# Kernel optimization log

Hardware: AMD Instinct MI355X
Metric: run time of the kernel (lower is better)

## Reference

```python
import jax, jax.numpy as jnp
import numpy as np

N_NODES, NUM_FEAT, EMB, HID, N_CLASSES, N_EDGES = 800, 111, 32, 200, 15, 8000
ALPHA = 0.5   # DirGNNConv default mixing
EPS = 1e-5    # LayerNorm eps


def _pade_coeffs(deg=5):
    # [5/5] Pade approximant of sqrt(1 - x) (as in FastDifferentiableMatSqrt)
    K = 2 * deg + 1
    b = np.zeros(K); b[0] = 1.0
    for k in range(1, K):
        b[k] = b[k - 1] * (0.5 - (k - 1)) / k
    c = b * ((-1.0) ** np.arange(K))  # Taylor coeffs of sqrt(1-x)
    A = np.empty((deg, deg))
    for i in range(deg):
        for j in range(1, deg + 1):
            A[i, j - 1] = c[deg + 1 + i - j]
    q = np.concatenate([[1.0], np.linalg.solve(A, -c[deg + 1:])])
    p = np.array([sum(q[j] * c[k - j] for j in range(min(k, deg) + 1)) for k in range(deg + 1)])
    return p.astype(np.float32), q.astype(np.float32)

PADE_P, PADE_Q = _pade_coeffs()


def _mpa_impl(A):
    # matrix square root via Pade approximant (MPA forward)
    normA = jnp.sqrt(jnp.sum(A * A))
    I = jnp.eye(A.shape[0], dtype=A.dtype)
    p_app = I - A / normA
    p_hat = p_app
    p_sqrt = PADE_P[0] * I
    q_sqrt = PADE_Q[0] * I
    for i in range(5):
        p_sqrt = p_sqrt + PADE_P[i + 1] * p_hat
        q_sqrt = q_sqrt + PADE_Q[i + 1] * p_hat
        p_hat = p_hat @ p_app
    return jnp.linalg.solve(q_sqrt, p_sqrt) * jnp.sqrt(normA)


@jax.custom_vjp
def mpa_lya(A):
    return _mpa_impl(A)


def _mpa_fwd(A):
    S = _mpa_impl(A)
    return S, (S, jnp.sqrt(jnp.sum(A * A)))


def _mpa_bwd(res, g):
    # iterative Lyapunov solver backward (8 coupled Newton-Schulz iterations)
    S, normA = res
    I = jnp.eye(S.shape[0], dtype=S.dtype)
    b = S / jnp.sqrt(normA)
    c = g / jnp.sqrt(normA)
    for _ in range(8):
        b2 = b @ b
        c = 0.5 * (c @ (3.0 * I - b2) - b2 @ c + b @ (c @ b))
        b = 0.5 * (b @ (3.0 * I - b2))
    return (0.5 * c,)

mpa_lya.defvjp(_mpa_fwd, _mpa_bwd)


def gcn_sparse(m, ei, n):
    # GCNConv(normalize=False): out[dst] = sum_{(src,dst) in E} (x @ W)[src]
    return jax.ops.segment_sum(m[ei[0]], ei[1], num_segments=n)


def hetero_layer_sparse(h, eis, W, b):
    # W: [3(in,out,root), 4 edge types, Fin, Fout]; HeteroConv aggr='sum'
    n = h.shape[0]
    out = jnp.zeros((n, W.shape[-1]), h.dtype)
    for e, ei in enumerate(eis):
        x_in = gcn_sparse(h @ W[0, e], ei, n) + b[0, e]
        x_out = gcn_sparse(h @ W[1, e], ei[::-1], n) + b[1, e]  # flipped edges
        out = out + ALPHA * x_out + (1.0 - ALPHA) * x_in + h @ W[2, e] + b[2, e]
    return out


def hetero_layer_dense(h, masks, W, b):
    # masks: [4, N, N] binary adjacency (src, dst); dense equivalent of scatter
    out = jnp.zeros((h.shape[0], W.shape[-1]), h.dtype)
    for e in range(masks.shape[0]):
        x_in = masks[e].T @ (h @ W[0, e]) + b[0, e]
        x_out = masks[e] @ (h @ W[1, e]) + b[1, e]
        out = out + ALPHA * x_out + (1.0 - ALPHA) * x_in + h @ W[2, e] + b[2, e]
    return out


def graph_layernorm(h, wb):
    # PyG LayerNorm mode='graph', single graph: normalize over all nodes+feats
    mu = jnp.mean(h)
    var = jnp.mean((h - mu) ** 2)
    return (h - mu) / jnp.sqrt(var + EPS) * wb[0] + wb[1]


def hetero_gnn(h, layer_fn, graph, W1, b1, W2, b2, ln):
    h = graph_layernorm(layer_fn(h, graph, W1, b1), ln[0])
    return graph_layernorm(layer_fn(h, graph, W2, b2), ln[1])


def pairwise_S(z, lin_W, lin_b, iu, ju):
    n = z.shape[0]
    M = (z[iu] - z[ju]) ** 2                        # [N(N+1)/2, HID]
    mg = jax.nn.sigmoid(M @ lin_W + lin_b)[:, 0]    # upper-tri entries, row-major
    tri = jnp.zeros((n, n), z.dtype).at[iu, ju].set(mg)
    return mpa_lya(tri)


def model_forward(x_note, embed_W, embed_b, g1_l1_W, g1_l1_b, g1_l2_W, g1_l2_b, g1_ln,
                  g2_l1_W, g2_l1_b, g2_l2_W, g2_l2_b, g2_ln, lin_W, lin_b, clf_W, clf_b,
                  eis, batch):
    n = x_note.shape[0]
    iu, ju = np.triu_indices(n)
    h = x_note @ embed_W + embed_b                   # [N, 32]
    z0 = hetero_gnn(h, hetero_layer_sparse, eis, g1_l1_W, g1_l1_b, g1_l2_W, g1_l2_b, g1_ln)
    S1 = pairwise_S(z0, lin_W, lin_b, iu, ju)
    A0 = jnp.stack([jnp.zeros((n, n), h.dtype).at[ei[0], ei[1]].set(1.0) for ei in eis])
    h = S1 @ h
    # adj_to_coord(nonzero) only keeps the binary pattern of S1 @ A @ S1
    mask1 = jnp.stack([((S1 @ A0[e]) @ S1 != 0).astype(h.dtype) for e in range(4)])
    z1 = hetero_gnn(h, hetero_layer_dense, mask1, g2_l1_W, g2_l1_b, g2_l2_W, g2_l2_b, g2_ln)
    S2 = pairwise_S(z1, lin_W, lin_b, iu, ju)
    h = S2 @ h
    mask2 = jnp.stack([((S2 @ mask1[e]) @ S2 != 0).astype(h.dtype) for e in range(4)])
    z2 = hetero_gnn(h, hetero_layer_dense, mask2, g2_l1_W, g2_l1_b, g2_l2_W, g2_l2_b, g2_ln)
    counts = jax.ops.segment_sum(jnp.ones((n,), z2.dtype), batch, num_segments=1)
    x2 = jax.ops.segment_sum(z2, batch, num_segments=1) / counts[:, None]  # global_mean_pool
    logits = x2 @ clf_W + clf_b
    return x2, jax.nn.log_softmax(logits, axis=-1), S1, S2


def setup_inputs() -> dict:
    key = jax.random.key(0)
    ks = jax.random.split(key, 14)
    N, F, E, H, NC, NE = N_NODES, NUM_FEAT, EMB, HID, N_CLASSES, N_EDGES
    def w(k, shape, fan_in):
        return (jax.random.normal(k, shape, jnp.float32) / np.sqrt(fan_in)).astype(jnp.float32)
    ln = jnp.broadcast_to(jnp.stack([jnp.ones(H, jnp.float32), jnp.zeros(H, jnp.float32)]), (2, 2, H)) + 0.0
    return dict(
        x_note=jax.random.normal(ks[0], (N, F), jnp.float32),
        embed_W=w(ks[1], (F, E), F), embed_b=jnp.zeros((E,), jnp.float32),
        g1_l1_W=w(ks[2], (3, 4, E, H), E), g1_l1_b=jnp.zeros((3, 4, H), jnp.float32),
        g1_l2_W=w(ks[3], (3, 4, H, H), H), g1_l2_b=jnp.zeros((3, 4, H), jnp.float32),
        g1_ln=ln,
        g2_l1_W=w(ks[4], (3, 4, E, H), E), g2_l1_b=jnp.zeros((3, 4, H), jnp.float32),
        g2_l2_W=w(ks[5], (3, 4, H, H), H), g2_l2_b=jnp.zeros((3, 4, H), jnp.float32),
        g2_ln=ln,
        lin_W=w(ks[6], (H, 1), H), lin_b=jnp.zeros((1,), jnp.float32),
        clf_W=w(ks[7], (H, NC), H), clf_b=jnp.zeros((NC,), jnp.float32),
        ei_forward=jax.random.randint(ks[8], (2, NE), 0, N, jnp.int32),
        ei_onset=jax.random.randint(ks[9], (2, NE), 0, N, jnp.int32),
        ei_sustain=jax.random.randint(ks[10], (2, NE), 0, N, jnp.int32),
        ei_rest=jax.random.randint(ks[11], (2, NE), 0, N, jnp.int32),
        batch=jnp.zeros((N,), jnp.int32),
    )


def reference(x_note, embed_W, embed_b, g1_l1_W, g1_l1_b, g1_l2_W, g1_l2_b, g1_ln,
              g2_l1_W, g2_l1_b, g2_l2_W, g2_l2_b, g2_ln, lin_W, lin_b, clf_W, clf_b,
              ei_forward, ei_onset, ei_sustain, ei_rest, batch):
    eis = (ei_forward, ei_onset, ei_sustain, ei_rest)
    return model_forward(x_note, embed_W, embed_b, g1_l1_W, g1_l1_b, g1_l2_W, g1_l2_b, g1_ln,
                         g2_l1_W, g2_l1_b, g2_l2_W, g2_l2_b, g2_ln, lin_W, lin_b, clf_W, clf_b,
                         eis, batch)
```

## Files before the change

### kernel.cpp

```cpp
#include <hip/hip_runtime.h>
#include <hip/hip_bf16.h>
#include <math.h>
#include <stdio.h>

static constexpr int   kN  = 800;
static constexpr int   kF  = 111;
static constexpr int   kE  = 32;
static constexpr int   kH  = 200;
static constexpr int   kNC = 15;
static constexpr int   kNE = 8000;
static constexpr long  kNN = (long)kN*kN;
static constexpr long  kNH = (long)kN*kH;
static constexpr float kAl  = 0.5f;
static constexpr float kEps = 1e-5f;
static constexpr int   kGB  = (int)((kNH+255)/256);
static constexpr int   kDB  = 50;
static constexpr int   kCH  = 50;
static constexpr int   kNCHK= kN/kCH;

typedef unsigned short u16;
typedef __attribute__((ext_vector_type(8))) short short8;
typedef __attribute__((ext_vector_type(4))) float f32x4;

__device__ __forceinline__ u16 f2bf(float v){
  __hip_bfloat16 b = __float2bfloat16(v);
  return *reinterpret_cast<u16*>(&b);
}
__device__ __forceinline__ float bf2f(u16 h){
  unsigned int u = ((unsigned int)h) << 16;
  float f; __builtin_memcpy(&f, &u, 4);
  return f;
}

enum { EPI_NONE=0, EPI_BIAS=1, EPI_SCALE=4, EPI_ACC=6 };

template<bool TRANSA, bool TRIUA, bool TRIUB, int EPI, bool LNA>
__global__ __launch_bounds__(256)
void gemm_kernel(const float* __restrict__ A, int lda,
                 const float* __restrict__ B, int ldb,
                 float* __restrict__ C, int ldc,
                 int M, int Ncl, int K,
                 long sA, long sB, long sC, float scale,
                 const float* __restrict__ bias, int kstep,
                 const double* __restrict__ scalp,
                 const float* __restrict__ lnw,
                 const double* __restrict__ lnpart, int lnnb)
{
  constexpr int TM=64, TN=64, TK=16;
  A += (long)blockIdx.z * sA;
  B += (long)blockIdx.z * sB;
  C += (long)blockIdx.z * sC;
  __shared__ float As[TK][TM+4];
  __shared__ float Bs[TK][TN+4];
  const int tid = threadIdx.x;
  const int tn4 = (tid & 15)*4, tm4 = (tid >> 4)*4;
  const int m0 = blockIdx.x * TM, n0 = blockIdx.y * TN;
  float acc[4][4] = {};
  float mu = 0.f, rsf = 1.f;
  if (LNA){
    __shared__ double lnS[256], lnQ[256];
    double s=0.0, q=0.0;
    for (int i=tid; i<lnnb; i+=256){ s += lnpart[2*i]; q += lnpart[2*i+1]; }
    lnS[tid]=s; lnQ[tid]=q;
    __syncthreads();
    for (int h=128; h>0; h>>=1){
      if (tid < h){ lnS[tid]+=lnS[tid+h]; lnQ[tid]+=lnQ[tid+h]; }
      __syncthreads();
    }
    double m = lnS[0]/(double)kNH;
    double var = lnQ[0]/(double)kNH - m*m;
    mu = (float)m;
    rsf = rsqrtf((float)var + kEps);
    __syncthreads();
  }
  const int kbase = kstep ? (int)blockIdx.z * kstep : 0;
  int k0 = TRIUA ? max(m0 - kbase, 0) : 0;
  int kEnd = TRIUB ? min(K, n0 + TN - kbase) : K;
  const bool skip = (k0 >= kEnd);
  if (skip && EPI == EPI_ACC) return;
  if (!skip) {
    float ar[4], br[4];
    auto loadT = [&](int kk0, float* arr, float* brr){
      #pragma unroll
      for (int u=0; u<4; ++u){
        int idx = tid + 256*u;
        float av = 0.f;
        if (!TRANSA) {
          int m = idx >> 4, ka = idx & 15;
          int gm = m0+m, gk = kk0+ka;
          if (gm < M && gk < K){
            av = A[(long)gm*lda + gk];
            if (LNA) av = (av - mu)*(rsf*lnw[gk]) + lnw[kH + gk];
          }
        } else {
          int ka = idx >> 6, m = idx & 63;
          int gm = m0+m, gk = kk0+ka;
          if (gm < M && gk < K){
            av = A[(long)gk*lda + gm];
            if (LNA) av = (av - mu)*(rsf*lnw[gk]) + lnw[kH + gk];
          }
        }
        int kb = idx >> 6, nb = idx & 63;
        int gk = kk0+kb, gn = n0+nb;
        arr[u] = av;
        brr[u] = (gk < K && gn < Ncl) ? B[(long)gk*ldb + gn] : 0.f;
      }
    };
    auto storeT = [&](const float* arr, const float* brr){
      #pragma unroll
      for (int u=0; u<4; ++u){
        int idx = tid + 256*u;
        if (!TRANSA){ int m = idx>>4, ka = idx&15; As[ka][m] = arr[u]; }
        else        { int ka = idx>>6, m = idx&63; As[ka][m] = arr[u]; }
        int kb = idx>>6, nb = idx&63;
        Bs[kb][nb] = brr[u];
      }
    };
    loadT(k0, ar, br);
    for (;;){
      __syncthreads();
      storeT(ar, br);
      __syncthreads();
      int kn = k0 + TK;
      bool more = kn < kEnd;
      if (more) loadT(kn, ar, br);
      #pragma unroll
      for (int kk=0; kk<TK; ++kk) {
        float a[4], b[4];
        #pragma unroll
        for (int u=0;u<4;++u){ a[u]=As[kk][tm4+u]; b[u]=Bs[kk][tn4+u]; }
        #pragma unroll
        for (int i=0;i<4;++i)
          #pragma unroll
          for (int j=0;j<4;++j)
            acc[i][j] = fmaf(a[i], b[j], acc[i][j]);
      }
      if (!more) break;
      k0 = kn;
    }
  }
  float sc = scale;
  if (EPI == EPI_ACC && scalp) sc *= (float)sqrt(sqrt(scalp[0]));
  #pragma unroll
  for (int i=0;i<4;++i) {
    int gm = m0 + tm4 + i;
    if (gm >= M) continue;
    #pragma unroll
    for (int j=0;j<4;++j) {
      int gn = n0 + tn4 + j;
      if (gn >= Ncl) continue;
      float v = acc[i][j];
      long off = (long)gm*ldc + gn;
      if (EPI == EPI_BIAS)       C[off] = v + bias[gn];
      else if (EPI == EPI_SCALE) C[off] = scale*v;
      else if (EPI == EPI_ACC)   unsafeAtomicAdd(&C[off], sc*v);
      else                       C[off] = v;
    }
  }
}

template<bool TRANSA, bool TRIUA, bool TRIUB, int EPI, bool LNA = false>
static inline void launch_gemm(hipStream_t st,
                               const float* A, int lda, const float* B, int ldb,
                               float* C, int ldc, int M, int Ncl, int K, int batch,
                               long sA, long sB, long sC, float scale,
                               const float* bias = nullptr, int kstep = 0,
                               const double* scalp = nullptr,
                               const float* lnw = nullptr,
                               const double* lnpart = nullptr, int lnnb = 0)
{
  dim3 grid((M+63)/64, (Ncl+63)/64, batch);
  gemm_kernel<TRANSA,TRIUA,TRIUB,EPI,LNA><<<grid, 256, 0, st>>>(
      A,lda,B,ldb,C,ldc,M,Ncl,K,sA,sB,sC,scale,bias,kstep,scalp,lnw,lnpart,lnnb);
}

__global__ __launch_bounds__(256)
void bgemm2_kernel(const u16* __restrict__ Ah, const u16* __restrict__ Al,
                   const u16* __restrict__ Bh, const u16* __restrict__ Bl,
                   float* __restrict__ C, float* __restrict__ C2,
                   u16* __restrict__ Oh, u16* __restrict__ Ol,
                   float p0, float p1)
{
  constexpr int TM=64, TN=64, BK=32;
  __shared__ u16 Ash[TM][40], Asl[TM][40], Bsh[TN][40], Bsl[TN][40];
  const int tid = threadIdx.x;
  const int m0 = blockIdx.x*TM, n0 = blockIdx.y*TN;
  const int w = tid>>6, lane = tid&63;
  const int wm = (w&1)*32, wn = (w>>1)*32;
  const int quad = lane>>4, lm = lane&15;
  f32x4 acc00={}, acc01={}, acc10={}, acc11={};
  const bool skip = (m0 > n0 + TN - 1);
  int k0 = m0;
  const int kEnd = min(kN, n0+TN);
  const int ar = tid>>2, ac = (tid&3)*8;
  if (!skip){
    uint4 avh, avl, bvh, bvl;
    auto loadT = [&](int kk0){
      avh = {0,0,0,0}; avl = {0,0,0,0}; bvh = {0,0,0,0}; bvl = {0,0,0,0};
      int gk = kk0 + ac;
      if (m0+ar < kN && gk < kN){
        avh = *(const uint4*)(Ah + (long)(m0+ar)*kN + gk);
        avl = *(const uint4*)(Al + (long)(m0+ar)*kN + gk);
      }
      if (n0+ar < kN && gk < kN){
        bvh = *(const uint4*)(Bh + (long)(n0+ar)*kN + gk);
        bvl = *(const uint4*)(Bl + (long)(n0+ar)*kN + gk);
      }
    };
    loadT(k0);
    for (;;){
      __syncthreads();
      *(uint4*)&Ash[ar][ac] = avh; *(uint4*)&Asl[ar][ac] = avl;
      *(uint4*)&Bsh[ar][ac] = bvh; *(uint4*)&Bsl[ar][ac] = bvl;
      __syncthreads();
      int kn = k0 + BK;
      bool more = kn < kEnd;
      if (more) loadT(kn);
      short8 a0h = *(const short8*)&Ash[wm+lm][quad*8];
      short8 a1h = *(const short8*)&Ash[wm+16+lm][quad*8];
      short8 a0l = *(const short8*)&Asl[wm+lm][quad*8];
      short8 a1l = *(const short8*)&Asl[wm+16+lm][quad*8];
      short8 b0h = *(const short8*)&Bsh[wn+lm][quad*8];
      short8 b1h = *(const short8*)&Bsh[wn+16+lm][quad*8];
      short8 b0l = *(const short8*)&Bsl[wn+lm][quad*8];
      short8 b1l = *(const short8*)&Bsl[wn+16+lm][quad*8];
      acc00 = __builtin_amdgcn_mfma_f32_16x16x32_bf16(a0h,b0h,acc00,0,0,0);
      acc00 = __builtin_amdgcn_mfma_f32_16x16x32_bf16(a0h,b0l,acc00,0,0,0);
      acc00 = __builtin_amdgcn_mfma_f32_16x16x32_bf16(a0l,b0h,acc00,0,0,0);
      acc01 = __builtin_amdgcn_mfma_f32_16x16x32_bf16(a0h,b1h,acc01,0,0,0);
      acc01 = __builtin_amdgcn_mfma_f32_16x16x32_bf16(a0h,b1l,acc01,0,0,0);
      acc01 = __builtin_amdgcn_mfma_f32_16x16x32_bf16(a0l,b1h,acc01,0,0,0);
      acc10 = __builtin_amdgcn_mfma_f32_16x16x32_bf16(a1h,b0h,acc10,0,0,0);
      acc10 = __builtin_amdgcn_mfma_f32_16x16x32_bf16(a1h,b0l,acc10,0,0,0);
      acc10 = __builtin_amdgcn_mfma_f32_16x16x32_bf16(a1l,b0h,acc10,0,0,0);
      acc11 = __builtin_amdgcn_mfma_f32_16x16x32_bf16(a1h,b1h,acc11,0,0,0);
      acc11 = __builtin_amdgcn_mfma_f32_16x16x32_bf16(a1h,b1l,acc11,0,0,0);
      acc11 = __builtin_amdgcn_mfma_f32_16x16x32_bf16(a1l,b1h,acc11,0,0,0);
      if (!more) break;
      k0 = kn;
    }
  }
  f32x4 accs[2][2] = {{acc00, acc01},{acc10, acc11}};
  #pragma unroll
  for (int ti=0; ti<2; ++ti){
    #pragma unroll
    for (int tj=0; tj<2; ++tj){
      #pragma unroll
      for (int r=0; r<4; ++r){
        int gm = m0 + wm + ti*16 + quad*4 + r;
        int gn = n0 + wn + tj*16 + lm;
        if (gm >= kN || gn >= kN) continue;
        float v = accs[ti][tj][r];
        long off = (long)gm*kN + gn;
        C[off]  += p0*v;
        C2[off] += p1*v;
        u16 h = f2bf(v);
        Oh[off] = h;
        Ol[off] = f2bf(v - bf2f(h));
      }
    }
  }
}

__global__ __launch_bounds__(256)
void ln_pair_prep_kernel(const float* __restrict__ tnh, const double* __restrict__ part,
                         int nb, const float* __restrict__ ln, const float* __restrict__ linW,
                         u16* __restrict__ zwh, u16* __restrict__ zwl,
                         u16* __restrict__ zzh, u16* __restrict__ zzl,
                         float* __restrict__ avec)
{
  __shared__ double ss[256], qq[256];
  __shared__ float ared[256];
  const int n = blockIdx.x, t = threadIdx.x;
  double s=0.0, q=0.0;
  for (int i=t; i<nb; i+=256){ s += part[2*i]; q += part[2*i+1]; }
  ss[t]=s; qq[t]=q;
  __syncthreads();
  for (int h=128; h>0; h>>=1){
    if (t < h){ ss[t]+=ss[t+h]; qq[t]+=qq[t+h]; }
    __syncthreads();
  }
  double m = ss[0]/(double)kNH;
  const float mu = (float)m;
  const float rs = rsqrtf((float)(qq[0]/(double)kNH - m*m) + kEps);
  float acc = 0.f;
  if (t < kH){
    float z = (tnh[(long)n*kH + t] - mu)*(rs*ln[t]) + ln[kH + t];
    float wv = linW[t];
    float zw = wv*z;
    long off = (long)n*kH + t;
    u16 h1 = f2bf(zw);
    zwh[off] = h1; zwl[off] = f2bf(zw - bf2f(h1));
    u16 h2 = f2bf(z);
    zzh[off] = h2; zzl[off] = f2bf(z - bf2f(h2));
    acc = zw*z;
  }
  ared[t] = acc;
  __syncthreads();
  for (int h=128; h>0; h>>=1){
    if (t < h) ared[t] += ared[t+h];
    __syncthreads();
  }
  if (t == 0) avec[n] = ared[0];
}

__global__ __launch_bounds__(256)
void bgemm_pair_kernel(const u16* __restrict__ Ah, const u16* __restrict__ Al,
                       const u16* __restrict__ Bh, const u16* __restrict__ Bl,
                       const float* __restrict__ avec, const float* __restrict__ linb,
                       float* __restrict__ tri, double* __restrict__ frob2)
{
  constexpr int TM=64, TN=64, BK=32, KK=kH;
  __shared__ u16 Ash[TM][40], Asl[TM][40], Bsh[TN][40], Bsl[TN][40];
  __shared__ float red[256];
  const int tid = threadIdx.x;
  const int m0 = blockIdx.x*TM, n0 = blockIdx.y*TN;
  if (m0 > n0 + TN - 1){
    for (int idx = tid; idx < TM*TN; idx += 256){
      int r = idx >> 6, c = idx & 63;
      int gm = m0 + r, gn = n0 + c;
      if (gm < kN && gn < kN) tri[(long)gm*kN + gn] = 0.f;
    }
    return;
  }
  const int w = tid>>6, lane = tid&63;
  const int wm = (w&1)*32, wn = (w>>1)*32;
// ... 50 lines not shown
        if (gm >= kN || gn >= kN) continue;
        float t = 0.f;
        if (gm <= gn){
          float marg = avec[gm] + avec[gn] - 2.f*accs[ti][tj][r] + lb;
          t = 1.f/(1.f + expf(-marg));
        }
        tri[(long)gm*kN + gn] = t;
        r2 += t*t;
      }
    }
  }
  red[tid] = r2;
  __syncthreads();
  for (int h=128; h>0; h>>=1){
    if (tid < h) red[tid] += red[tid+h];
    __syncthreads();
  }
  if (tid == 0) unsafeAtomicAdd(frob2, (double)red[0]);
}

__global__ __launch_bounds__(256)
void pade_both_kernel(const float* __restrict__ tri, const double* __restrict__ frob2,
                      u16* __restrict__ ph, u16* __restrict__ pl,
                      u16* __restrict__ th, u16* __restrict__ tl,
                      float* __restrict__ psq, float* __restrict__ qsq,
                      float P0, float P1, float Q0, float Q1)
{
  __shared__ float t[32][33];
  const float rn = (float)(1.0 / sqrt(frob2[0]));
  int r0 = blockIdx.y*32, c0 = blockIdx.x*32;
  int tr = threadIdx.x>>5, tc = threadIdx.x&31;
  for (int i=tr; i<32; i+=8){
    int r = r0+i, c = c0+tc;
    float eye = (r==c) ? 1.f : 0.f;
    float pa = eye - tri[(long)r*kN + c]*rn;
    t[i][tc] = pa;
    long off = (long)r*kN + c;
    psq[off] = P0*eye + P1*pa;
    qsq[off] = Q0*eye + Q1*pa;
    u16 h = f2bf(pa);
    ph[off] = h;
    pl[off] = f2bf(pa - bf2f(h));
  }
  __syncthreads();
  for (int i=tr; i<32; i+=8){
    int c = c0+i, r = r0+tc;
    float v = t[tc][i];
    u16 h = f2bf(v);
    th[(long)c*kN + r] = h;
    tl[(long)c*kN + r] = f2bf(v - bf2f(h));
  }
}

__global__ __launch_bounds__(256)
void copy_scale_kernel(const float* __restrict__ src, const double* __restrict__ frob2,
                       float* __restrict__ dst)
{
  const float fac = (float)sqrt(sqrt(frob2[0]));
  long i = (long)blockIdx.x*256 + threadIdx.x;
  if (i < kNN) __builtin_nontemporal_store(src[i]*fac, &dst[i]);
}

__global__ void edge_count_kernel(const int* __restrict__ e0, const int* __restrict__ e1,
                                  const int* __restrict__ e2, const int* __restrict__ e3,
                                  int* __restrict__ cnt){
  const int* eis[4] = {e0,e1,e2,e3};
  const int e = blockIdx.y;
  const int* ei = eis[e];
  int j = blockIdx.x*256 + threadIdx.x;
  if (j >= kNE) return;
  int s = ei[j], d = ei[kNE + j];
  atomicAdd(&cnt[e*kN + d], 1);
  atomicAdd(&cnt[(4+e)*kN + s], 1);
}

__global__ void csr_scan_kernel(const int* __restrict__ cnt, int* __restrict__ offs,
                                int* __restrict__ cur){
  const int l = blockIdx.x;
  if (threadIdx.x != 0) return;
  int acc = 0;
  for (int i = 0; i < kN; ++i){
    offs[l*(kN+1) + i] = acc;
    cur[l*kN + i] = acc;
    acc += cnt[l*kN + i];
  }
  offs[l*(kN+1) + kN] = acc;
}

__global__ void edge_fill_kernel(const int* __restrict__ e0, const int* __restrict__ e1,
                                 const int* __restrict__ e2, const int* __restrict__ e3,
                                 int* __restrict__ cur, int* __restrict__ adj){
  const int* eis[4] = {e0,e1,e2,e3};
  const int e = blockIdx.y;
  const int* ei = eis[e];
  int j = blockIdx.x*256 + threadIdx.x;
  if (j >= kNE) return;
  int s = ei[j], d = ei[kNE + j];
  int p = atomicAdd(&cur[e*kN + d], 1);
  adj[(long)e*kNE + p] = s;
  int q = atomicAdd(&cur[(4+e)*kN + s], 1);
  adj[(long)(4+e)*kNE + q] = d;
}

__global__ __launch_bounds__(256)
void gather_sparse_kernel(const float* __restrict__ Y, const int* __restrict__ offs,
                          const int* __restrict__ adj, const float* __restrict__ bsum,
                          float* __restrict__ tnh, double* __restrict__ part){
  __shared__ double ss[256], qq[256];
  const int n = blockIdx.x;
  const int f = threadIdx.x;
  double sp = 0.0, qp = 0.0;
  float acc = 0.f;
  if (f < kH){
    #pragma unroll
    for (int l = 0; l < 8; ++l){
      const float* Yp = Y + (long)l*kNH;
      int b = offs[l*(kN+1) + n], e2 = offs[l*(kN+1) + n + 1];
      for (int idx = b; idx < e2; ++idx){
        int m = adj[(long)l*kNE + idx];
        acc += Yp[(long)m*kH + f];
      }
    }
    float t = Y[(long)8*kNH + (long)n*kH + f] + bsum[f] + 0.5f*acc;
    tnh[(long)n*kH + f] = t;
    sp = t; qp = (double)t*t;
  }
  ss[threadIdx.x]=sp; qq[threadIdx.x]=qp;
  __syncthreads();
  for (int hh=128; hh>0; hh>>=1){
    if ((int)threadIdx.x < hh){ ss[threadIdx.x]+=ss[threadIdx.x+hh]; qq[threadIdx.x]+=qq[threadIdx.x+hh]; }
    __syncthreads();
  }
  if (threadIdx.x==0){ part[2*blockIdx.x]=ss[0]; part[2*blockIdx.x+1]=qq[0]; }
}

__global__ void edge_gmax_kernel(const int* __restrict__ e0, const int* __restrict__ e1,
                                 const int* __restrict__ e2, const int* __restrict__ e3,
                                 int* __restrict__ g){
  const int* eis[4] = {e0,e1,e2,e3};
  const int e = blockIdx.y;
  const int* ei = eis[e];
  int j = blockIdx.x*256 + threadIdx.x;
  if (j >= kNE) return;
  int s = ei[j], d = ei[kNE + j];
  atomicMax(&g[e*kN + d], s);
}

__global__ __launch_bounds__(256)
void scan_gh_kernel(int* __restrict__ g, int* __restrict__ h){
  __shared__ int gs[kN];
  const int e = blockIdx.x;
  for (int i = threadIdx.x; i < kN; i += 256) gs[i] = g[e*kN + i];
  __syncthreads();
  if (threadIdx.x == 0){
    int m = -1;
    for (int i = 0; i < kN; ++i){ m = max(m, gs[i]); gs[i] = m; }
  }
  __syncthreads();
  for (int i = threadIdx.x; i < kN; i += 256) g[e*kN + i] = gs[i];
  for (int d = threadIdx.x; d < kN; d += 256){
    int lo = 0, hi = kN;
    while (lo < hi){ int mid = (lo+hi)>>1; if (gs[mid] >= d) hi = mid; else lo = mid+1; }
    h[e*kN + d] = lo;
  }
}

__global__ __launch_bounds__(256)
void scan_chunk_kernel(float* __restrict__ Y, float* __restrict__ Tot){
  const int plane = blockIdx.y;
  const int chunk = blockIdx.x;
  const int f = threadIdx.x;
  if (f >= kH) return;
  float* P = Y + (long)plane*kNH + (long)chunk*kCH*kH + f;
  float acc = 0.f;
  if (plane < 4){
    for (int i0 = 0; i0 < kCH; i0 += 5){
      float v0 = P[(long)(i0+0)*kH], v1 = P[(long)(i0+1)*kH], v2 = P[(long)(i0+2)*kH],
            v3 = P[(long)(i0+3)*kH], v4 = P[(long)(i0+4)*kH];
      acc += v0; P[(long)(i0+0)*kH] = acc;
      acc += v1; P[(long)(i0+1)*kH] = acc;
      acc += v2; P[(long)(i0+2)*kH] = acc;
      acc += v3; P[(long)(i0+3)*kH] = acc;
      acc += v4; P[(long)(i0+4)*kH] = acc;
    }
  } else {
    for (int i0 = kCH-1; i0 >= 4; i0 -= 5){
      float v0 = P[(long)(i0-0)*kH], v1 = P[(long)(i0-1)*kH], v2 = P[(long)(i0-2)*kH],
            v3 = P[(long)(i0-3)*kH], v4 = P[(long)(i0-4)*kH];
      acc += v0; P[(long)(i0-0)*kH] = acc;
      acc += v1; P[(long)(i0-1)*kH] = acc;
      acc += v2; P[(long)(i0-2)*kH] = acc;
      acc += v3; P[(long)(i0-3)*kH] = acc;
      acc += v4; P[(long)(i0-4)*kH] = acc;
    }
  }
  Tot[((long)plane*kNCHK + chunk)*kH + f] = acc;
}

__global__ __launch_bounds__(256)
void gather_dense_kernel(const float* __restrict__ Y, const int* __restrict__ g,
                         const int* __restrict__ h, const float* __restrict__ bsum,
                         const float* __restrict__ Tot,
                         float* __restrict__ tnh, double* __restrict__ part){
  __shared__ double ss[256], qq[256];
  long idx = (long)blockIdx.x*256 + threadIdx.x;
  double s = 0.0, q = 0.0;
  if (idx < kNH){
    int n = (int)(idx / kH), f = (int)(idx % kH);
    float v = 0.f;
    #pragma unroll
    for (int e = 0; e < 4; ++e){
      int gi = g[e*kN + n];
      if (gi >= 0){
        v += Y[(long)e*kNH + (long)gi*kH + f];
        int cg = (int)((unsigned)gi / (unsigned)kCH);
        const float* T = Tot + (long)e*kNCHK*kH + f;
        for (int cc = 0; cc < cg; ++cc) v += T[(long)cc*kH];
      }
      int hi = h[e*kN + n];
      if (hi < kN){
        v += Y[(long)(4+e)*kNH + (long)hi*kH + f];
        int ch = (int)((unsigned)hi / (unsigned)kCH);
        const float* T = Tot + (long)(4+e)*kNCHK*kH + f;
        for (int cc = ch+1; cc < kNCHK; ++cc) v += T[(long)cc*kH];
      }
    }
    float t = Y[(long)8*kNH + idx] + bsum[f] + 0.5f*v;
    tnh[idx] = t;
    s = t; q = (double)t*t;
  }
  ss[threadIdx.x]=s; qq[threadIdx.x]=q;
  __syncthreads();
  for (int hh=128; hh>0; hh>>=1){
    if ((int)threadIdx.x < hh){ ss[threadIdx.x]+=ss[threadIdx.x+hh]; qq[threadIdx.x]+=qq[threadIdx.x+hh]; }
    __syncthreads();
  }
  if (threadIdx.x==0){ part[2*blockIdx.x]=ss[0]; part[2*blockIdx.x+1]=qq[0]; }
}

__global__ void sum_root_kernel(const float* __restrict__ W, const float* __restrict__ b,
                                int K, float* __restrict__ Wr, float* __restrict__ bsum){
  int idx = blockIdx.x*256 + threadIdx.x;
  int tot = K*kH;
  if (idx < tot){
    float v = 0.f;
    #pragma unroll
    for (int e=0;e<4;++e) v += W[(long)(8+e)*tot + idx];
    Wr[idx] = v;
  }
  if (idx < kH){
    float v = 0.f;
    #pragma unroll
    for (int e=0;e<4;++e)
      v += (1.f-kAl)*b[(0*4+e)*kH + idx] + kAl*b[(1*4+e)*kH + idx] + b[(2*4+e)*kH + idx];
    bsum[idx] = v;
  }
}

__global__ __launch_bounds__(64)
void invdiag_kernel(const float* __restrict__ U, float* __restrict__ W){
  __shared__ float Us[kDB][kDB+1];
  __shared__ float Xs[kDB][kDB+1];
  const int base = blockIdx.x * kDB;
  const int tid = threadIdx.x;
  for (int idx = tid; idx < kDB*kDB; idx += 64){
    int r = idx / kDB, c = idx % kDB;
    Us[r][c] = U[(long)(base+r)*kN + base + c];
  }
  __syncthreads();
  const int c = tid;
  for (int i = kDB-1; i >= 0; --i){
    if (c < kDB){
      float x;
      if (c < i) x = 0.f;
      else {
        float s = 0.f;
        for (int k = i+1; k < kDB; ++k) s = fmaf(Us[i][k], Xs[k][c], s);
        x = (((c==i)?1.f:0.f) - s) / Us[i][i];
      }
      Xs[i][c] = x;
    }
    __syncthreads();
  }
  for (int idx = tid; idx < kDB*kDB; idx += 64){
    int r = idx / kDB, cc = idx % kDB;
    W[(long)(base+r)*kN + base + cc] = Xs[r][cc];
  }
}

template<int S>
__global__ __launch_bounds__(256)
void merge_fused_kernel(const float* __restrict__ U, float* __restrict__ W){
  __shared__ float Us[S][S+1];
  __shared__ float Wb[S][S+1];
  __shared__ float T[S][S+1];
  const long base = (long)blockIdx.x * (2*S) * (kN+1);
  const int tid = threadIdx.x;
  for (int idx = tid; idx < S*S; idx += 256){
    int r = idx / S, c = idx % S;
    Us[r][c] = U[base + (long)r*kN + S + c];
    Wb[r][c] = W[base + (long)(S+r)*kN + S + c];
  }
  __syncthreads();
  for (int idx = tid; idx < S*S; idx += 256){
    int r = idx / S, c = idx % S;
    float s = 0.f;
    for (int k = 0; k <= c; ++k) s = fmaf(Us[r][k], Wb[k][c], s);
    T[r][c] = s;
  }
// ... 164 lines not shown
  double* scald = (double*)d_ws;
  double* partd = (double*)((char*)d_ws + 512);
  float *h0=ws+o_h0, *h1=ws+o_h1, *h2=ws+o_h2, *tnh=ws+o_tnh,
        *big=ws+o_big, *tri=ws+o_tri, *Sacc=ws+o_sacc, *winv=ws+o_winv,
        *psq=ws+o_psq, *qsq=ws+o_qsq;
  u16* zwh = (u16*)(ws + o_pp);
  u16* zwl = zwh + kNH;
  u16* zzh = zwl + kNH;
  u16* zzl = zzh + kNH;
  float* avec = ws + o_av;
  int* gArr = (int*)(ws + o_g);
  int* hArr = (int*)(ws + o_hh);
  float *wc1=ws+o_wc1, *wc2=ws+o_wc2, *wc3=ws+o_wc3, *wc4=ws+o_wc4, *bs=ws+o_bs;
  int* cntA = (int*)(ws + o_cnt);
  int* offsA= (int*)(ws + o_offs);
  int* curA = (int*)(ws + o_cur);
  int* adjA = (int*)(ws + o_adj);
  u16* papp_h = (u16*)big;
  u16* papp_l = papp_h + kNN;
  u16* pT_h   = papp_l + kNN;
  u16* pT_l   = pT_h + kNN;
  u16* pwA_h  = pT_l + kNN;
  u16* pwA_l  = pwA_h + kNN;
  u16* pwB_h  = pwA_l + kNN;
  u16* pwB_l  = pwB_h + kNN;
  float* totbuf  = big + (long)9*kNH;
  float* colpart = totbuf + (long)8*kNCHK*kH;

  float P[6], Q[6];
  pade_coeffs(P, Q);

  auto eg = [](long n){ return dim3((unsigned)((n+255)/256)); };

  auto layer_gemm = [&](const float* hin, int K, const float* wcat,
                        const float* lnp, int nb){
    if (lnp)
      launch_gemm<false,false,false,EPI_NONE,true>(stream, hin, K, wcat, kH, big, kH,
          kN, kH, K, 9, 0, (long)K*kH, kNH, 0.f, nullptr, 0, nullptr, lnp, partd, nb);
    else
      launch_gemm<false,false,false,EPI_NONE>(stream, hin, K, wcat, kH, big, kH,
          kN, kH, K, 9, 0, (long)K*kH, kNH, 0.f);
  };
  auto sparse_layer = [&](const float* hin, int K, const float* wcat, const float* bsum,
                          const float* lnp, int nb){
    layer_gemm(hin, K, wcat, lnp, nb);
    gather_sparse_kernel<<<dim3(kN),256,0,stream>>>(big, offsA, adjA, bsum, tnh, partd);
  };
  auto dense_layer = [&](const float* hin, int K, const float* wcat, const float* bsum,
                         const float* lnp, int nb){
    layer_gemm(hin, K, wcat, lnp, nb);
    scan_chunk_kernel<<<dim3(kNCHK,8),256,0,stream>>>(big, totbuf);
    gather_dense_kernel<<<kGB,256,0,stream>>>(big, gArr, hArr, bsum, totbuf, tnh, partd);
  };
  auto blocked_trsm = [&](){
    hipMemsetAsync(winv, 0, (size_t)kNN*sizeof(float), stream);
    invdiag_kernel<<<dim3(kN/kDB),64,0,stream>>>(qsq, winv);
    merge_fused_kernel<50><<<dim3(kN/100),256,0,stream>>>(qsq, winv);
    {
      int s = 100, npairs = 4;
      long step = (long)2*s*kN + 2*s;
      launch_gemm<false,false,true,EPI_NONE>(stream,
          qsq + s, kN, winv + (long)s*kN + s, kN, tri, s,
          s, s, s, npairs, step, step, (long)s*s, 0.f);
      launch_gemm<false,true,false,EPI_SCALE>(stream,
          winv, kN, tri, s, winv + s, kN,
          s, s, s, npairs, step, (long)s*s, step, -1.f);
    }
    {
      int s = 200, npairs = 2;
      long step = (long)2*s*kN + 2*s;
      launch_gemm<false,false,true,EPI_NONE>(stream,
          qsq + s, kN, winv + (long)s*kN + s, kN, tri, s,
          s, s, s, npairs, step, step, (long)s*s, 0.f);
      launch_gemm<false,true,false,EPI_SCALE>(stream,
          winv, kN, tri, s, winv + s, kN,
          s, s, s, npairs, step, (long)s*s, step, -1.f);
    }
    {
      hipMemsetAsync(tri, 0, (size_t)400*400*sizeof(float), stream);
      launch_gemm<false,false,true,EPI_ACC>(stream,
          qsq + 400, kN, winv + (long)400*kN + 400, kN, tri, 400,
          400, 400, 100, 4, 100, (long)100*kN, 0, 1.f, nullptr, 100);
      launch_gemm<false,true,false,EPI_ACC>(stream,
          winv, kN, tri, 400, winv + 400, kN,
          400, 400, 100, 4, 100, (long)100*400, 0, -1.f, nullptr, 100);
    }
    hipMemsetAsync(Sacc, 0, (size_t)kNN*sizeof(float), stream);
    launch_gemm<false,true,true,EPI_ACC>(stream,
        winv, kN, psq, kN, Sacc, kN, kN, kN, 100, 8,
        100, (long)100*kN, 0, 1.f, nullptr, 100);
  };
  auto run_pair_mpa = [&](int nb, const float* lnp, float* SoutDst){
    hipMemsetAsync((char*)d_ws + 24, 0, 8, stream);
    ln_pair_prep_kernel<<<dim3(kN),256,0,stream>>>(tnh, partd, nb, lnp, linW,
                                                   zwh, zwl, zzh, zzl, avec);
    bgemm_pair_kernel<<<dim3(13,13),256,0,stream>>>(zwh, zwl, zzh, zzl, avec, linb,
                                                    tri, scald+3);
    pade_both_kernel<<<dim3(25,25),256,0,stream>>>(tri, scald+3, papp_h, papp_l, pT_h, pT_l,
                                                   psq, qsq, P[0],P[1],Q[0],Q[1]);
    dim3 g13(13,13,1);
    bgemm2_kernel<<<g13,256,0,stream>>>(papp_h,papp_l, pT_h,pT_l, psq,qsq, pwA_h,pwA_l, P[2],Q[2]);
    bgemm2_kernel<<<g13,256,0,stream>>>(pwA_h,pwA_l,  pT_h,pT_l, psq,qsq, pwB_h,pwB_l, P[3],Q[3]);
    bgemm2_kernel<<<g13,256,0,stream>>>(pwB_h,pwB_l,  pT_h,pT_l, psq,qsq, pwA_h,pwA_l, P[4],Q[4]);
    bgemm2_kernel<<<g13,256,0,stream>>>(pwA_h,pwA_l,  pT_h,pT_l, psq,qsq, pwB_h,pwB_l, P[5],Q[5]);
    blocked_trsm();
    copy_scale_kernel<<<eg(kNN),256,0,stream>>>(Sacc, scald+3, SoutDst);
  };
  auto s_times_h = [&](const float* hin, float* hout){
    hipMemsetAsync(hout, 0, (size_t)kN*kE*sizeof(float), stream);
    launch_gemm<false,true,false,EPI_ACC>(stream,
        Sacc, kN, hin, kE, hout, kE, kN, kE, 100, 8,
        100, (long)100*kE, 0, 1.f, nullptr, 100, scald+3);
  };

  float* S1f = out + 215;
  float* S2f = out + 215 + kNN;

  hipMemsetAsync(gArr, 0xFF, (size_t)(4*kN)*sizeof(int), stream);
  edge_gmax_kernel<<<dim3((kNE+255)/256,4),256,0,stream>>>(e0,e1,e2,e3, gArr);
  scan_gh_kernel<<<4,256,0,stream>>>(gArr, hArr);
  hipMemsetAsync(cntA, 0, (size_t)(8*kN)*sizeof(int), stream);
  edge_count_kernel<<<dim3((kNE+255)/256,4),256,0,stream>>>(e0,e1,e2,e3, cntA);
  csr_scan_kernel<<<8,64,0,stream>>>(cntA, offsA, curA);
  edge_fill_kernel<<<dim3((kNE+255)/256,4),256,0,stream>>>(e0,e1,e2,e3, curA, adjA);
  hipMemcpyAsync(wc1, g1w1, 8L*kE*kH*sizeof(float), hipMemcpyDeviceToDevice, stream);
  hipMemcpyAsync(wc2, g1w2, 8L*kH*kH*sizeof(float), hipMemcpyDeviceToDevice, stream);
  hipMemcpyAsync(wc3, g2w1, 8L*kE*kH*sizeof(float), hipMemcpyDeviceToDevice, stream);
  hipMemcpyAsync(wc4, g2w2, 8L*kH*kH*sizeof(float), hipMemcpyDeviceToDevice, stream);
  sum_root_kernel<<<eg((long)kE*kH),256,0,stream>>>(g1w1, g1b1, kE, wc1 + 8L*kE*kH, bs);
  sum_root_kernel<<<eg((long)kH*kH),256,0,stream>>>(g1w2, g1b2, kH, wc2 + 8L*kH*kH, bs+kH);
  sum_root_kernel<<<eg((long)kE*kH),256,0,stream>>>(g2w1, g2b1, kE, wc3 + 8L*kE*kH, bs+2*kH);
  sum_root_kernel<<<eg((long)kH*kH),256,0,stream>>>(g2w2, g2b2, kH, wc4 + 8L*kH*kH, bs+3*kH);

  launch_gemm<false,false,false,EPI_BIAS>(stream, x_note, kF, embW, kE, h0, kE, kN, kE, kF, 1,
                                          0,0,0, 0.f, embB);

  sparse_layer(h0,  kE, wc1, bs,      nullptr, 0);
  sparse_layer(tnh, kH, wc2, bs+kH,   g1ln, kN);

  run_pair_mpa(kN, g1ln + 2*kH, S1f);

  s_times_h(h0, h1);

  dense_layer(h1,  kE, wc3, bs+2*kH, nullptr, 0);
  dense_layer(tnh, kH, wc4, bs+3*kH, g2ln, kGB);

  run_pair_mpa(kGB, g2ln + 2*kH, S2f);

  s_times_h(h1, h2);

  dense_layer(h2,  kE, wc3, bs+2*kH, nullptr, 0);
  dense_layer(tnh, kH, wc4, bs+3*kH, g2ln, kGB);

  colsum_kernel<<<dim3(50),256,0,stream>>>(tnh, colpart);
  pool_head_kernel<<<dim3(1),256,0,stream>>>(colpart, partd, kGB, g2ln + 2*kH, clfW, clfb, out);
}
```

Before: 1.068 ms.

## Fuse setup kernels, drop memsets, and replace split-K atomics with direct GEMM stores

Merges weight copies, root-weight sums, bias combining and buffer initialisation into one prep kernel. The edge count and gmax kernels become one, and the two scans become one. Split-K atomic GEMMs in the triangular solve and S·h products become single-pass GEMMs with plain or scaled stores, so their memsets go away. The final S GEMM writes both the raw and scaled outputs, which removes the copy-scale kernel and the unused last bf16 split store. Together this cuts kernel launches and atomic traffic, but each single-pass GEMM now has fewer blocks and so less parallelism. The winv memset is hoisted to run once, which relies on its zero regions never being written in between.

```diff
diff --git a/kernel.cpp b/kernel.cpp
--- a/kernel.cpp
+++ b/kernel.cpp
@@ -32,7 +32,7 @@
   return f;
 }
 
-enum { EPI_NONE=0, EPI_BIAS=1, EPI_SCALE=4, EPI_ACC=6 };
+enum { EPI_NONE=0, EPI_BIAS=1, EPI_SCALE=4, EPI_ACC=6, EPI_DUAL=7 };
 
 template<bool TRANSA, bool TRIUA, bool TRIUB, int EPI, bool LNA>
 __global__ __launch_bounds__(256)
@@ -44,7 +44,8 @@
                  const float* __restrict__ bias, int kstep,
                  const double* __restrict__ scalp,
                  const float* __restrict__ lnw,
-                 const double* __restrict__ lnpart, int lnnb)
+                 const double* __restrict__ lnpart, int lnnb,
+                 float* __restrict__ C2)
 {
   constexpr int TM=64, TN=64, TK=16;
   A += (long)blockIdx.z * sA;
@@ -140,7 +141,8 @@
     }
   }
   float sc = scale;
-  if (EPI == EPI_ACC && scalp) sc *= (float)sqrt(sqrt(scalp[0]));
+  if ((EPI == EPI_ACC || EPI == EPI_SCALE || EPI == EPI_DUAL) && scalp)
+    sc *= (float)sqrt(sqrt(scalp[0]));
   #pragma unroll
   for (int i=0;i<4;++i) {
     int gm = m0 + tm4 + i;
@@ -152,8 +154,9 @@
       float v = acc[i][j];
       long off = (long)gm*ldc + gn;
       if (EPI == EPI_BIAS)       C[off] = v + bias[gn];
-      else if (EPI == EPI_SCALE) C[off] = scale*v;
+      else if (EPI == EPI_SCALE) C[off] = sc*v;
       else if (EPI == EPI_ACC)   unsafeAtomicAdd(&C[off], sc*v);
+      else if (EPI == EPI_DUAL){ C[off] = v; C2[off] = sc*v; }
       else                       C[off] = v;
     }
   }
@@ -167,11 +170,12 @@
                                const float* bias = nullptr, int kstep = 0,
                                const double* scalp = nullptr,
                                const float* lnw = nullptr,
-                               const double* lnpart = nullptr, int lnnb = 0)
+                               const double* lnpart = nullptr, int lnnb = 0,
+                               float* C2 = nullptr)
 {
   dim3 grid((M+63)/64, (Ncl+63)/64, batch);
   gemm_kernel<TRANSA,TRIUA,TRIUB,EPI,LNA><<<grid, 256, 0, st>>>(
-      A,lda,B,ldb,C,ldc,M,Ncl,K,sA,sB,sC,scale,bias,kstep,scalp,lnw,lnpart,lnnb);
+      A,lda,B,ldb,C,ldc,M,Ncl,K,sA,sB,sC,scale,bias,kstep,scalp,lnw,lnpart,lnnb,C2);
 }
 
 __global__ __launch_bounds__(256)
@@ -254,9 +258,11 @@
         long off = (long)gm*kN + gn;
         C[off]  += p0*v;
         C2[off] += p1*v;
-        u16 h = f2bf(v);
-        Oh[off] = h;
-        Ol[off] = f2bf(v - bf2f(h));
+        if (Oh){
+          u16 h = f2bf(v);
+          Oh[off] = h;
+          Ol[off] = f2bf(v - bf2f(h));
+        }
       }
     }
   }
@@ -267,11 +273,12 @@
                          int nb, const float* __restrict__ ln, const float* __restrict__ linW,
                          u16* __restrict__ zwh, u16* __restrict__ zwl,
                          u16* __restrict__ zzh, u16* __restrict__ zzl,
-                         float* __restrict__ avec)
+                         float* __restrict__ avec, double* __restrict__ frobz)
 {
   __shared__ double ss[256], qq[256];
   __shared__ float ared[256];
   const int n = blockIdx.x, t = threadIdx.x;
+  if (t == 0) *frobz = 0.0;
   double s=0.0, q=0.0;
   for (int i=t; i<nb; i+=256){ s += part[2*i]; q += part[2*i+1]; }
   ss[t]=s; qq[t]=q;
@@ -428,18 +435,64 @@
   }
 }
 
-__global__ __launch_bounds__(256)
-void copy_scale_kernel(const float* __restrict__ src, const double* __restrict__ frob2,
-                       float* __restrict__ dst)
+__device__ __forceinline__ float bias_comb(const float* __restrict__ b, int i){
+  float v = 0.f;
+  #pragma unroll
+  for (int e=0;e<4;++e)
+    v += (1.f-kAl)*b[(0*4+e)*kH + i] + kAl*b[(1*4+e)*kH + i] + b[(2*4+e)*kH + i];
+  return v;
+}
+
+__global__ __launch_bounds__(256)
+void prep_kernel(const float* __restrict__ g1w1, const float* __restrict__ g1b1,
+                 const float* __restrict__ g1w2, const float* __restrict__ g1b2,
+                 const float* __restrict__ g2w1, const float* __restrict__ g2b1,
+                 const float* __restrict__ g2w2, const float* __restrict__ g2b2,
+                 float* __restrict__ wc1, float* __restrict__ wc2,
+                 float* __restrict__ wc3, float* __restrict__ wc4,
+                 float* __restrict__ bs, int* __restrict__ cnt, int* __restrict__ g)
 {
-  const float fac = (float)sqrt(sqrt(frob2[0]));
+  constexpr int EH = kE*kH, HH = kH*kH;
   long i = (long)blockIdx.x*256 + threadIdx.x;
-  if (i < kNN) __builtin_nontemporal_store(src[i]*fac, &dst[i]);
-}
-
-__global__ void edge_count_kernel(const int* __restrict__ e0, const int* __restrict__ e1,
-                                  const int* __restrict__ e2, const int* __restrict__ e3,
-                                  int* __restrict__ cnt){
+  if (i < 8L*EH){ wc1[i] = g1w1[i]; return; } i -= 8L*EH;
+  if (i < EH){
+    float v=0.f;
+    #pragma unroll
+    for (int e=0;e<4;++e) v += g1w1[(long)(8+e)*EH + i];
+    wc1[8L*EH+i] = v; return;
+  } i -= EH;
+  if (i < 8L*HH){ wc2[i] = g1w2[i]; return; } i -= 8L*HH;
+  if (i < HH){
+    float v=0.f;
+    #pragma unroll
+    for (int e=0;e<4;++e) v += g1w2[(long)(8+e)*HH + i];
+    wc2[8L*HH+i] = v; return;
+  } i -= HH;
+  if (i < 8L*EH){ wc3[i] = g2w1[i]; return; } i -= 8L*EH;
+  if (i < EH){
+    float v=0.f;
+    #pragma unroll
+    for (int e=0;e<4;++e) v += g2w1[(long)(8+e)*EH + i];
+    wc3[8L*EH+i] = v; return;
+  } i -= EH;
+  if (i < 8L*HH){ wc4[i] = g2w2[i]; return; } i -= 8L*HH;
+  if (i < HH){
+    float v=0.f;
+    #pragma unroll
+    for (int e=0;e<4;++e) v += g2w2[(long)(8+e)*HH + i];
+    wc4[8L*HH+i] = v; return;
+  } i -= HH;
+  if (i < kH){ bs[i]        = bias_comb(g1b1, (int)i); return; } i -= kH;
+  if (i < kH){ bs[kH+i]     = bias_comb(g1b2, (int)i); return; } i -= kH;
+  if (i < kH){ bs[2*kH+i]   = bias_comb(g2b1, (int)i); return; } i -= kH;
+  if (i < kH){ bs[3*kH+i]   = bias_comb(g2b2, (int)i); return; } i -= kH;
+  if (i < 8L*kN){ cnt[i] = 0; return; } i -= 8L*kN;
+  if (i < 4L*kN){ g[i] = -1; return; }
+}
+
+__global__ void edge_cg_kernel(const int* __restrict__ e0, const int* __restrict__ e1,
+                               const int* __restrict__ e2, const int* __restrict__ e3,
+                               int* __restrict__ cnt, int* __restrict__ g){
   const int* eis[4] = {e0,e1,e2,e3};
   const int e = blockIdx.y;
   const int* ei = eis[e];
@@ -448,19 +501,41 @@
   int s = ei[j], d = ei[kNE + j];
   atomicAdd(&cnt[e*kN + d], 1);
   atomicAdd(&cnt[(4+e)*kN + s], 1);
-}
-
-__global__ void csr_scan_kernel(const int* __restrict__ cnt, int* __restrict__ offs,
-                                int* __restrict__ cur){
-  const int l = blockIdx.x;
-  if (threadIdx.x != 0) return;
-  int acc = 0;
-  for (int i = 0; i < kN; ++i){
-    offs[l*(kN+1) + i] = acc;
-    cur[l*kN + i] = acc;
-    acc += cnt[l*kN + i];
-  }
-  offs[l*(kN+1) + kN] = acc;
+  atomicMax(&g[e*kN + d], s);
+}
+
+__global__ __launch_bounds__(256)
+void scan12_kernel(const int* __restrict__ cnt, int* __restrict__ offs, int* __restrict__ cur,
+                   int* __restrict__ g, int* __restrict__ h){
+  __shared__ int buf[kN+1];
+  const int b = blockIdx.x, t = threadIdx.x;
+  if (b < 8){
+    for (int i=t; i<kN; i+=256) buf[i] = cnt[b*kN + i];
+    __syncthreads();
+    if (t == 0){
+      int acc = 0;
+      for (int i=0;i<kN;++i){ int c = buf[i]; buf[i] = acc; acc += c; }
+      buf[kN] = acc;
+    }
+    __syncthreads();
+    for (int i=t; i<kN; i+=256){ offs[b*(kN+1)+i] = buf[i]; cur[b*kN+i] = buf[i]; }
+    if (t == 0) offs[b*(kN+1)+kN] = buf[kN];
+  } else {
+    const int e = b - 8;
+    for (int i=t; i<kN; i+=256) buf[i] = g[e*kN + i];
+    __syncthreads();
+    if (t == 0){
+      int m = -1;
+      for (int i=0;i<kN;++i){ m = max(m, buf[i]); buf[i] = m; }
+    }
+    __syncthreads();
+    for (int i=t; i<kN; i+=256) g[e*kN + i] = buf[i];
+    for (int d=t; d<kN; d+=256){
+      int lo = 0, hi = kN;
+      while (lo < hi){ int mid = (lo+hi)>>1; if (buf[mid] >= d) hi = mid; else lo = mid+1; }
+      h[e*kN + d] = lo;
+    }
+  }
 }
 
 __global__ void edge_fill_kernel(const int* __restrict__ e0, const int* __restrict__ e1,
@@ -508,37 +583,6 @@
     __syncthreads();
   }
   if (threadIdx.x==0){ part[2*blockIdx.x]=ss[0]; part[2*blockIdx.x+1]=qq[0]; }
-}
-
-__global__ void edge_gmax_kernel(const int* __restrict__ e0, const int* __restrict__ e1,
-                                 const int* __restrict__ e2, const int* __restrict__ e3,
-                                 int* __restrict__ g){
-  const int* eis[4] = {e0,e1,e2,e3};
-  const int e = blockIdx.y;
-  const int* ei = eis[e];
-  int j = blockIdx.x*256 + threadIdx.x;
-  if (j >= kNE) return;
-  int s = ei[j], d = ei[kNE + j];
-  atomicMax(&g[e*kN + d], s);
-}
-
-__global__ __launch_bounds__(256)
-void scan_gh_kernel(int* __restrict__ g, int* __restrict__ h){
-  __shared__ int gs[kN];
-  const int e = blockIdx.x;
-  for (int i = threadIdx.x; i < kN; i += 256) gs[i] = g[e*kN + i];
-  __syncthreads();
-  if (threadIdx.x == 0){
-    int m = -1;
-    for (int i = 0; i < kN; ++i){ m = max(m, gs[i]); gs[i] = m; }
-  }
-  __syncthreads();
-  for (int i = threadIdx.x; i < kN; i += 256) g[e*kN + i] = gs[i];
-  for (int d = threadIdx.x; d < kN; d += 256){
-    int lo = 0, hi = kN;
-    while (lo < hi){ int mid = (lo+hi)>>1; if (gs[mid] >= d) hi = mid; else lo = mid+1; }
-    h[e*kN + d] = lo;
-  }
 }
 
 __global__ __launch_bounds__(256)
@@ -612,25 +656,6 @@
     __syncthreads();
   }
   if (threadIdx.x==0){ part[2*blockIdx.x]=ss[0]; part[2*blockIdx.x+1]=qq[0]; }
-}
-
-__global__ void sum_root_kernel(const float* __restrict__ W, const float* __restrict__ b,
-                                int K, float* __restrict__ Wr, float* __restrict__ bsum){
-  int idx = blockIdx.x*256 + threadIdx.x;
-  int tot = K*kH;
-  if (idx < tot){
-    float v = 0.f;
-    #pragma unroll
-    for (int e=0;e<4;++e) v += W[(long)(8+e)*tot + idx];
-    Wr[idx] = v;
-  }
-  if (idx < kH){
-    float v = 0.f;
-    #pragma unroll
-    for (int e=0;e<4;++e)
-      v += (1.f-kAl)*b[(0*4+e)*kH + idx] + kAl*b[(1*4+e)*kH + idx] + b[(2*4+e)*kH + idx];
-    bsum[idx] = v;
-  }
 }
 
 __global__ __launch_bounds__(64)
@@ -901,8 +926,7 @@
     scan_chunk_kernel<<<dim3(kNCHK,8),256,0,stream>>>(big, totbuf);
     gather_dense_kernel<<<kGB,256,0,stream>>>(big, gArr, hArr, bsum, totbuf, tnh, partd);
   };
-  auto blocked_trsm = [&](){
-    hipMemsetAsync(winv, 0, (size_t)kNN*sizeof(float), stream);
+  auto blocked_trsm = [&](float* SoutDst){
     invdiag_kernel<<<dim3(kN/kDB),64,0,stream>>>(qsq, winv);
     merge_fused_kernel<50><<<dim3(kN/100),256,0,stream>>>(qsq, winv);
     {
@@ -926,23 +950,20 @@
           s, s, s, npairs, step, (long)s*s, step, -1.f);
     }
     {
-      hipMemsetAsync(tri, 0, (size_t)400*400*sizeof(float), stream);
-      launch_gemm<false,false,true,EPI_ACC>(stream,
+      launch_gemm<false,false,true,EPI_NONE>(stream,
           qsq + 400, kN, winv + (long)400*kN + 400, kN, tri, 400,
-          400, 400, 100, 4, 100, (long)100*kN, 0, 1.f, nullptr, 100);
-      launch_gemm<false,true,false,EPI_ACC>(stream,
+          400, 400, 400, 1, 0, 0, 0, 0.f);
+      launch_gemm<false,true,false,EPI_SCALE>(stream,
           winv, kN, tri, 400, winv + 400, kN,
-          400, 400, 100, 4, 100, (long)100*400, 0, -1.f, nullptr, 100);
-    }
-    hipMemsetAsync(Sacc, 0, (size_t)kNN*sizeof(float), stream);
-    launch_gemm<false,true,true,EPI_ACC>(stream,
-        winv, kN, psq, kN, Sacc, kN, kN, kN, 100, 8,
-        100, (long)100*kN, 0, 1.f, nullptr, 100);
+          400, 400, 400, 1, 0, 0, 0, -1.f);
+    }
+    launch_gemm<false,true,true,EPI_DUAL>(stream,
+        winv, kN, psq, kN, Sacc, kN, kN, kN, kN, 1,
+        0, 0, 0, 1.f, nullptr, 0, scald+3, nullptr, nullptr, 0, SoutDst);
   };
   auto run_pair_mpa = [&](int nb, const float* lnp, float* SoutDst){
-    hipMemsetAsync((char*)d_ws + 24, 0, 8, stream);
     ln_pair_prep_kernel<<<dim3(kN),256,0,stream>>>(tnh, partd, nb, lnp, linW,
-                                                   zwh, zwl, zzh, zzl, avec);
+                                                   zwh, zwl, zzh, zzl, avec, scald+3);
     bgemm_pair_kernel<<<dim3(13,13),256,0,stream>>>(zwh, zwl, zzh, zzl, avec, linb,
                                                     tri, scald+3);
     pade_both_kernel<<<dim3(25,25),256,0,stream>>>(tri, scald+3, papp_h, papp_l, pT_h, pT_l,
@@ -951,35 +972,28 @@
     bgemm2_kernel<<<g13,256,0,stream>>>(papp_h,papp_l, pT_h,pT_l, psq,qsq, pwA_h,pwA_l, P[2],Q[2]);
     bgemm2_kernel<<<g13,256,0,stream>>>(pwA_h,pwA_l,  pT_h,pT_l, psq,qsq, pwB_h,pwB_l, P[3],Q[3]);
     bgemm2_kernel<<<g13,256,0,stream>>>(pwB_h,pwB_l,  pT_h,pT_l, psq,qsq, pwA_h,pwA_l, P[4],Q[4]);
-    bgemm2_kernel<<<g13,256,0,stream>>>(pwA_h,pwA_l,  pT_h,pT_l, psq,qsq, pwB_h,pwB_l, P[5],Q[5]);
-    blocked_trsm();
-    copy_scale_kernel<<<eg(kNN),256,0,stream>>>(Sacc, scald+3, SoutDst);
+    bgemm2_kernel<<<g13,256,0,stream>>>(pwA_h,pwA_l,  pT_h,pT_l, psq,qsq, nullptr,nullptr, P[5],Q[5]);
+    blocked_trsm(SoutDst);
   };
   auto s_times_h = [&](const float* hin, float* hout){
-    hipMemsetAsync(hout, 0, (size_t)kN*kE*sizeof(float), stream);
-    launch_gemm<false,true,false,EPI_ACC>(stream,
-        Sacc, kN, hin, kE, hout, kE, kN, kE, 100, 8,
-        100, (long)100*kE, 0, 1.f, nullptr, 100, scald+3);
+    launch_gemm<false,true,false,EPI_SCALE>(stream,
+        Sacc, kN, hin, kE, hout, kE, kN, kE, kN, 1,
+        0, 0, 0, 1.f, nullptr, 0, scald+3);
   };
 
   float* S1f = out + 215;
   float* S2f = out + 215 + kNN;
 
-  hipMemsetAsync(gArr, 0xFF, (size_t)(4*kN)*sizeof(int), stream);
-  edge_gmax_kernel<<<dim3((kNE+255)/256,4),256,0,stream>>>(e0,e1,e2,e3, gArr);
-  scan_gh_kernel<<<4,256,0,stream>>>(gArr, hArr);
-  hipMemsetAsync(cntA, 0, (size_t)(8*kN)*sizeof(int), stream);
-  edge_count_kernel<<<dim3((kNE+255)/256,4),256,0,stream>>>(e0,e1,e2,e3, cntA);
-  csr_scan_kernel<<<8,64,0,stream>>>(cntA, offsA, curA);
+  hipMemsetAsync(winv, 0, (size_t)kNN*sizeof(float), stream);
+  {
+    constexpr long prep_span = 2L*(9L*kE*kH + 9L*kH*kH) + 4L*kH + 8L*kN + 4L*kN;
+    prep_kernel<<<eg(prep_span),256,0,stream>>>(g1w1, g1b1, g1w2, g1b2,
+                                                g2w1, g2b1, g2w2, g2b2,
+                                                wc1, wc2, wc3, wc4, bs, cntA, gArr);
+  }
+  edge_cg_kernel<<<dim3((kNE+255)/256,4),256,0,stream>>>(e0,e1,e2,e3, cntA, gArr);
+  scan12_kernel<<<dim3(12),256,0,stream>>>(cntA, offsA, curA, gArr, hArr);
   edge_fill_kernel<<<dim3((kNE+255)/256,4),256,0,stream>>>(e0,e1,e2,e3, curA, adjA);
-  hipMemcpyAsync(wc1, g1w1, 8L*kE*kH*sizeof(float), hipMemcpyDeviceToDevice, stream);
-  hipMemcpyAsync(wc2, g1w2, 8L*kH*kH*sizeof(float), hipMemcpyDeviceToDevice, stream);
-  hipMemcpyAsync(wc3, g2w1, 8L*kE*kH*sizeof(float), hipMemcpyDeviceToDevice, stream);
-  hipMemcpyAsync(wc4, g2w2, 8L*kH*kH*sizeof(float), hipMemcpyDeviceToDevice, stream);
-  sum_root_kernel<<<eg((long)kE*kH),256,0,stream>>>(g1w1, g1b1, kE, wc1 + 8L*kE*kH, bs);
-  sum_root_kernel<<<eg((long)kH*kH),256,0,stream>>>(g1w2, g1b2, kH, wc2 + 8L*kH*kH, bs+kH);
-  sum_root_kernel<<<eg((long)kE*kH),256,0,stream>>>(g2w1, g2b1, kE, wc3 + 8L*kE*kH, bs+2*kH);
-  sum_root_kernel<<<eg((long)kH*kH),256,0,stream>>>(g2w2, g2b2, kH, wc4 + 8L*kH*kH, bs+3*kH);
 
   launch_gemm<false,false,false,EPI_BIAS>(stream, x_note, kF, embW, kE, h0, kE, kN, kE, kF, 1,
                                           0,0,0, 0.f, embB);
```

Measured after the change: 1.151 ms. 1.08x slower.
